# Optimization experiments

Measured on AMD Instinct MI355X. Metric: run time of the kernel, lower is better.

The kernel has to match this reference:

```python
import jax, jax.numpy as jnp
import numpy as np

NU, NI, C, E, L = 100000, 50000, 128, 1000000, 200000
TAU = 0.05  # SemanticUpdateWA weight on past embeddings


def setup_inputs() -> dict:
    key = jax.random.key(0)
    ks = jax.random.split(key, 40)
    it = iter(ks)
    f = lambda shape, s=1.0: jax.random.normal(next(it), shape, jnp.float32) * s
    inp = {}
    inp['x_user'] = f((NU, C))
    inp['x_item'] = f((NI, C))
    inp['past1_user'] = f((NU, C))
    inp['past1_item'] = f((NI, C))
    inp['past2_user'] = f((NU, C))
    inp['past2_item'] = f((NI, C))
    w = 0.05  # param scale
    for nm, shp in [('W1ui_n', (C, C)), ('W1ui_s', (C, C)), ('W1iu_n', (C, C)), ('W1iu_s', (C, C)),
                    ('Wp1', (C, C)), ('bp1', (C,)), ('Wa1', (C, C)), ('ba1', (C,)), ('q1', (C,)),
                    ('W2ui_n', (C, C)), ('W2ui_s', (C, C)), ('W2iu_n', (C, C)), ('W2iu_s', (C, C)),
                    ('Wp2', (C, C)), ('bp2', (C,)), ('Wa2', (C, C)), ('ba2', (C,)), ('q2', (C,)),
                    ('Wpost', (C, 2)), ('bpost', (2,))]:
        inp[nm] = f(shp, w)
    inp['src_ui'] = jax.random.randint(next(it), (E,), 0, NU)
    inp['dst_ui'] = jax.random.randint(next(it), (E,), 0, NI)
    inp['src_iu'] = jax.random.randint(next(it), (E,), 0, NI)
    inp['dst_iu'] = jax.random.randint(next(it), (E,), 0, NU)
    inp['lbl_src'] = jax.random.randint(next(it), (L,), 0, NU)
    inp['lbl_dst'] = jax.random.randint(next(it), (L,), 0, NI)
    inp['snap'] = 1
    return inp


def _seg_mean(src_feat, src, dst, n_dst):
    # mean-aggregated messages: gather src features along edges, scatter-mean to dst
    msg = src_feat[src]                                   # [E, C]
    s = jax.ops.segment_sum(msg, dst, num_segments=n_dst)  # [n_dst, C]
    cnt = jax.ops.segment_sum(jnp.ones((src.shape[0], 1), src_feat.dtype), dst, num_segments=n_dst)
    return s / jnp.maximum(cnt, 1.0)


def _sem_agg(z, W, b, q):
    # HAN-style semantic attention over relations. z: [N, R, C]
    w = jnp.einsum('nrc,c->nr', jnp.tanh(jnp.einsum('nrc,cd->nrd', z, W) + b), q).mean(axis=0)  # [R]
    beta = jax.nn.softmax(w)
    return jnp.einsum('nrc,r->nc', z, beta)


def reference(x_user, x_item, past1_user, past1_item, past2_user, past2_item,
              W1ui_n, W1ui_s, W1iu_n, W1iu_s, Wp1, bp1, Wa1, ba1, q1,
              W2ui_n, W2ui_s, W2iu_n, W2iu_s, Wp2, bp2, Wa2, ba2, q2,
              Wpost, bpost,
              src_ui, dst_ui, src_iu, dst_iu, lbl_src, lbl_dst, snap):
    # --- layer 1: per-relation heterogeneous conv (GraphConv-style: W_n*mean_aggr + W_s*x_self) ---
    item1 = _seg_mean(x_user, src_ui, dst_ui, NI) @ W1ui_n + x_item @ W1ui_s
    user1 = _seg_mean(x_item, src_iu, dst_iu, NU) @ W1iu_n + x_user @ W1iu_s
    user1 = user1 @ Wp1 + bp1                              # projuser1
    if snap != 0:                                          # temporal weighted-average update
        user1 = TAU * past1_user + (1.0 - TAU) * user1
        item1 = TAU * past1_item + (1.0 - TAU) * item1
    cur1_user, cur1_item = user1, item1
    user_h = _sem_agg(user1[:, None, :], Wa1, ba1, q1)     # semantic aggregation (R=1 per type)
    item_h = _sem_agg(item1[:, None, :], Wa1, ba1, q1)
    # --- layer 2 ---
    item2 = _seg_mean(user_h, src_ui, dst_ui, NI) @ W2ui_n + item_h @ W2ui_s
    user2 = _seg_mean(item_h, src_iu, dst_iu, NU) @ W2iu_n + user_h @ W2iu_s
    user2 = user2 @ Wp2 + bp2                              # projuser2
    if snap != 0:
        user2 = TAU * past2_user + (1.0 - TAU) * user2
        item2 = TAU * past2_item + (1.0 - TAU) * item2
    cur2_user, cur2_item = user2, item2
    user_o = _sem_agg(user2[:, None, :], Wa2, ba2, q2)
    item_o = _sem_agg(item2[:, None, :], Wa2, ba2, q2)
    # --- link scoring: gather, Hadamard, linear, sum ---
    h = ((user_o[lbl_src] * item_o[lbl_dst]) @ Wpost + bpost).sum(axis=-1)  # [L]
    return (h, cur1_user, cur1_item, cur2_user, cur2_item)
```

## Files before the change

kernel.cpp:

```cpp
#include <hip/hip_runtime.h>


#define NUSER 100000
#define NITEM 50000
#define CDIM  128
#define EDGES 1000000
#define LBL   200000

#define OFF_C1U ((long)LBL)
#define OFF_C1I (OFF_C1U + (long)NUSER * CDIM)
#define OFF_C2U (OFF_C1I + (long)NITEM * CDIM)
#define OFF_C2I (OFF_C2U + (long)NUSER * CDIM)

typedef __bf16 bf16x8 __attribute__((ext_vector_type(8)));
typedef float  f32x4  __attribute__((ext_vector_type(4)));

__device__ __forceinline__ float ld1(const void* base, size_t idx, bool isf32) {
  return isf32 ? ((const float*)base)[idx] : (float)((const __bf16*)base)[idx];
}

__global__ void probe_dtype_kernel(const unsigned short* __restrict__ x,
                                   int* __restrict__ flag) {
  int t = threadIdx.x;
  int bad = 0;
  for (int i = t * 2; i < 8192; i += 512) {
    int e = (x[i] >> 7) & 0xFF;
    if (e > 0x85) bad = 1;
  }
  if (bad) atomicOr(flag, 1);
}

__global__ __launch_bounds__(256) void hist_kernel(
    const int* __restrict__ dst_ui, const int* __restrict__ dst_iu,
    int* __restrict__ cntI, int* __restrict__ cntU) {
  int e = blockIdx.x * 256 + threadIdx.x;
  if (e < EDGES) {
    atomicAdd(&cntI[dst_ui[e]], 1);
    atomicAdd(&cntU[dst_iu[e]], 1);
  }
}

__global__ __launch_bounds__(1024) void scan2_kernel(
    const int* __restrict__ cntI, int* __restrict__ offI, int* __restrict__ curI,
    int nI, const int* __restrict__ cntU, int* __restrict__ offU,
    int* __restrict__ curU, int nU) {
  const int* cnt = blockIdx.x ? cntU : cntI;
  int* off = blockIdx.x ? offU : offI;
  int* cur = blockIdx.x ? curU : curI;
  int n = blockIdx.x ? nU : nI;
  __shared__ int wsums[16];
  __shared__ int carry_s;
  int t = threadIdx.x, lane = t & 63, w = t >> 6;
  if (t == 0) carry_s = 0;
  __syncthreads();
  for (int base = 0; base < n; base += 1024) {
    int i = base + t;
    int v = (i < n) ? cnt[i] : 0;
    int x = v;
#pragma unroll
    for (int s = 1; s < 64; s <<= 1) {
      int y = __shfl_up(x, s, 64);
      if (lane >= s) x += y;
    }
    if (lane == 63) wsums[w] = x;
    __syncthreads();
    int woff = 0;
    for (int ww = 0; ww < w; ++ww) woff += wsums[ww];
    int carry = carry_s;
    __syncthreads();
    int excl = carry + woff + x - v;
    if (i < n) { off[i] = excl; cur[i] = excl; }
    if (t == 1023) carry_s = excl + v;
    __syncthreads();
  }
  if (t == 0) off[n] = carry_s;
}

__global__ __launch_bounds__(256) void bucket_kernel(
    const int* __restrict__ src_ui, const int* __restrict__ dst_ui,
    const int* __restrict__ src_iu, const int* __restrict__ dst_iu,
    int* __restrict__ curI, int* __restrict__ curU,
    int* __restrict__ permI, int* __restrict__ permU) {
  int e = blockIdx.x * 256 + threadIdx.x;
  if (e < EDGES) {
    int p = atomicAdd(&curI[dst_ui[e]], 1);
    permI[p] = src_ui[e];
    int p2 = atomicAdd(&curU[dst_iu[e]], 1);
    permU[p2] = src_iu[e];
  }
}

__global__ __launch_bounds__(256) void convert_bf16_kernel(
    const void* __restrict__ in, __bf16* __restrict__ outp, long n,
    const int* __restrict__ flag) {
  bool f = flag[0] != 0;
  long i = ((long)blockIdx.x * 256 + threadIdx.x) * 8;
  if (i + 8 > n) return;
  bf16x8 o;
  if (f) {
    f32x4 a = *(const f32x4*)((const float*)in + i);
    f32x4 b = *(const f32x4*)((const float*)in + i + 4);
#pragma unroll
    for (int j = 0; j < 4; ++j) {
      o[j] = (__bf16)a[j];
      o[4 + j] = (__bf16)b[j];
    }
  } else {
    o = *(const bf16x8*)((const __bf16*)in + i);
  }
  *(bf16x8*)(outp + i) = o;
}

__global__ __launch_bounds__(128) void prep_transpose_kernel(
    const void* __restrict__ W0, const void* __restrict__ W1,
    const void* __restrict__ W2, const void* __restrict__ W3,
    __bf16* __restrict__ T0, __bf16* __restrict__ T1,
    __bf16* __restrict__ T2, __bf16* __restrict__ T3,
    const int* __restrict__ flag) {
  bool f = flag[0] != 0;
  int k = blockIdx.x, n = threadIdx.x, y = blockIdx.y;
  const void* W = (y == 0) ? W0 : (y == 1) ? W1 : (y == 2) ? W2 : W3;
  __bf16* T = (y == 0) ? T0 : (y == 1) ? T1 : (y == 2) ? T2 : T3;
  T[n * CDIM + k] = (__bf16)ld1(W, (size_t)k * CDIM + n, f);
}

__global__ __launch_bounds__(128) void prep_combine_kernel(
    const void* __restrict__ W0, const void* __restrict__ W1,
    const void* __restrict__ W2, const void* __restrict__ W3,
    const void* __restrict__ Wp1, const void* __restrict__ Wp2,
    __bf16* __restrict__ T0, __bf16* __restrict__ T1,
    __bf16* __restrict__ T2, __bf16* __restrict__ T3,
    const int* __restrict__ flag) {
  bool f = flag[0] != 0;
  int k = blockIdx.x, n = threadIdx.x, y = blockIdx.y;
  const void* W = (y == 0) ? W0 : (y == 1) ? W1 : (y == 2) ? W2 : W3;
  const void* Wp = (y < 2) ? Wp1 : Wp2;
  __bf16* T = (y == 0) ? T0 : (y == 1) ? T1 : (y == 2) ? T2 : T3;
  float s = 0.f;
#pragma unroll 4
  for (int j = 0; j < CDIM; ++j)
    s += ld1(W, (size_t)k * CDIM + j, f) * ld1(Wp, (size_t)j * CDIM + n, f);
  T[n * CDIM + k] = (__bf16)s;
}

__global__ void prep_misc_kernel(const void* __restrict__ Wpost,
                                 const void* __restrict__ bpost,
                                 const void* __restrict__ bp1,
                                 const void* __restrict__ bp2,
                                 float* __restrict__ wsum,
                                 float* __restrict__ bpf1,
                                 float* __restrict__ bpf2,
                                 const int* __restrict__ flag) {
  bool f = flag[0] != 0;
  int t = threadIdx.x;
  wsum[t] = ld1(Wpost, (size_t)t * 2, f) + ld1(Wpost, (size_t)t * 2 + 1, f);
  bpf1[t] = ld1(bp1, t, f);
  bpf2[t] = ld1(bp2, t, f);
  if (t == 0) wsum[CDIM] = ld1(bpost, 0, f) + ld1(bpost, 1, f);
}

template <bool HAS_BIAS>
__global__ __launch_bounds__(256, 4) void gather_gemm_coop(
    const int* __restrict__ off, const int* __restrict__ perm,
    const __bf16* __restrict__ feat, const __bf16* __restrict__ X,
    const __bf16* __restrict__ WtN, const __bf16* __restrict__ WtS,
    const float* __restrict__ bias, const void* __restrict__ past,
    __bf16* __restrict__ shadow_out, const int* __restrict__ snapp,
    const int* __restrict__ flag, void* __restrict__ outb, long outoff,
    int nRowTiles) {
  __shared__ float lds[4][16][132];
  float* ldsOut = &lds[0][0][0];
  bool f32o = (flag[0] != 0);
  bool blend = (snapp[0] != 0);
  int t = threadIdx.x;
  int w = t >> 6, lane = t & 63, ln = lane & 15, q = lane >> 4;
  int cq = q * 8;
  for (int rt = blockIdx.x; rt < nRowTiles; rt += gridDim.x) {
    int row = rt * 16 + ln;
    int beg = off[row], end = off[row + 1];
    int cnt = end - beg;
    int myBeg = beg + ((cnt * w) >> 2);
    int myEnd = beg + ((cnt * (w + 1)) >> 2);
    float s[4][8];
#pragma unroll
    for (int a = 0; a < 4; ++a)
#pragma unroll
      for (int j = 0; j < 8; ++j) s[a][j] = 0.f;
    {
      const __bf16* fb = feat + cq;
      int i = myBeg;
      for (; i + 1 < myEnd; i += 2) {
        const __bf16* fp0 = fb + (size_t)perm[i] * CDIM;
        const __bf16* fp1 = fb + (size_t)perm[i + 1] * CDIM;
        bf16x8 v0[4], v1[4];
#pragma unroll
        for (int ks = 0; ks < 4; ++ks) v0[ks] = *(const bf16x8*)(fp0 + ks * 32);
#pragma unroll
        for (int ks = 0; ks < 4; ++ks) v1[ks] = *(const bf16x8*)(fp1 + ks * 32);
#pragma unroll
        for (int ks = 0; ks < 4; ++ks)
#pragma unroll
          for (int j = 0; j < 8; ++j)
            s[ks][j] += (float)v0[ks][j] + (float)v1[ks][j];
      }
      if (i < myEnd) {
        const __bf16* fp = fb + (size_t)perm[i] * CDIM;
#pragma unroll
        for (int ks = 0; ks < 4; ++ks) {
          bf16x8 v = *(const bf16x8*)(fp + ks * 32);
#pragma unroll
          for (int j = 0; j < 8; ++j) s[ks][j] += (float)v[j];
        }
      }
    }
#pragma unroll
    for (int ks = 0; ks < 4; ++ks) {
      *(f32x4*)&lds[w][ln][cq + ks * 32] =
          (f32x4){s[ks][0], s[ks][1], s[ks][2], s[ks][3]};
      *(f32x4*)&lds[w][ln][cq + ks * 32 + 4] =
          (f32x4){s[ks][4], s[ks][5], s[ks][6], s[ks][7]};
    }
    __syncthreads();
    float rc = 1.0f / fmaxf((float)cnt, 1.0f);
    bf16x8 a1[4], a2[4];
#pragma unroll
    for (int ks = 0; ks < 4; ++ks) {
      f32x4 lo = (f32x4){0.f, 0.f, 0.f, 0.f};
      f32x4 hi = (f32x4){0.f, 0.f, 0.f, 0.f};
#pragma unroll
      for (int w2 = 0; w2 < 4; ++w2) {
        const float* p = &lds[w2][ln][cq + ks * 32];
        lo += *(const f32x4*)p;
        hi += *(const f32x4*)(p + 4);
      }
      bf16x8 t1;
#pragma unroll
      for (int j = 0; j < 4; ++j) {
        t1[j] = (__bf16)(lo[j] * rc);
        t1[4 + j] = (__bf16)(hi[j] * rc);
      }
      a1[ks] = t1;
      a2[ks] = *(const bf16x8*)(X + (size_t)row * CDIM + cq + ks * 32);
    }
    f32x4 d0 = (f32x4){0.f, 0.f, 0.f, 0.f};
    f32x4 d1 = (f32x4){0.f, 0.f, 0.f, 0.f};
    const __bf16* bn0 = WtN + (size_t)((2 * w) * 16 + ln) * CDIM + cq;
    const __bf16* bs0 = WtS + (size_t)((2 * w) * 16 + ln) * CDIM + cq;
#pragma unroll
    for (int ks = 0; ks < 4; ++ks) {
      d0 = __builtin_amdgcn_mfma_f32_16x16x32_bf16(
          a1[ks], *(const bf16x8*)(bn0 + ks * 32), d0, 0, 0, 0);
      d0 = __builtin_amdgcn_mfma_f32_16x16x32_bf16(
          a2[ks], *(const bf16x8*)(bs0 + ks * 32), d0, 0, 0, 0);
      d1 = __builtin_amdgcn_mfma_f32_16x16x32_bf16(
          a1[ks], *(const bf16x8*)(bn0 + 16 * CDIM + ks * 32), d1, 0, 0, 0);
      d1 = __builtin_amdgcn_mfma_f32_16x16x32_bf16(
          a2[ks], *(const bf16x8*)(bs0 + 16 * CDIM + ks * 32), d1, 0, 0, 0);
    }
    __syncthreads();
#pragma unroll
    for (int p = 0; p < 2; ++p) {
      f32x4 dd = p ? d1 : d0;
      int col = (2 * w + p) * 16 + ln;
      float bv = HAS_BIAS ? bias[col] : 0.0f;
#pragma unroll
      for (int r = 0; r < 4; ++r)
        ldsOut[(q * 4 + r) * 132 + col] = dd[r] + bv;
    }
    __syncthreads();
    {
      int orow16 = t >> 4, c0 = (t & 15) * 8;
      long orow = (long)rt * 16 + orow16;
      const float* lp = ldsOut + orow16 * 132 + c0;
      f32x4 v0 = *(const f32x4*)lp;
      f32x4 v1 = *(const f32x4*)(lp + 4);
      if (blend) {
        if (f32o) {
          const float* pp = (const float*)past + orow * CDIM + c0;
          f32x4 p0 = *(const f32x4*)pp;
          f32x4 p1 = *(const f32x4*)(pp + 4);
#pragma unroll
          for (int j = 0; j < 4; ++j) {
            v0[j] = 0.05f * p0[j] + 0.95f * v0[j];
            v1[j] = 0.05f * p1[j] + 0.95f * v1[j];
          }
        } else {
          bf16x8 pb =
              *(const bf16x8*)((const __bf16*)past + orow * CDIM + c0);
#pragma unroll
          for (int j = 0; j < 4; ++j) {
            v0[j] = 0.05f * (float)pb[j] + 0.95f * v0[j];
            v1[j] = 0.05f * (float)pb[4 + j] + 0.95f * v1[j];
          }
        }
      }
      if (shadow_out) {
        bf16x8 sh;
#pragma unroll
        for (int j = 0; j < 4; ++j) {
          sh[j] = (__bf16)v0[j];
          sh[4 + j] = (__bf16)v1[j];
        }
        *(bf16x8*)(shadow_out + orow * CDIM + c0) = sh;
      }
      if (f32o) {
        float* op = (float*)outb + outoff + orow * CDIM + c0;
        *(f32x4*)op = v0;
        *(f32x4*)(op + 4) = v1;
      } else {
        bf16x8 ob;
#pragma unroll
        for (int j = 0; j < 4; ++j) {
          ob[j] = (__bf16)v0[j];
          ob[4 + j] = (__bf16)v1[j];
        }
        *(bf16x8*)((__bf16*)outb + outoff + orow * CDIM + c0) = ob;
      }
    }
    __syncthreads();
  }
}

template <bool HAS_BIAS>
__global__ __launch_bounds__(256) void gather_gemm_kernel(
    const int* __restrict__ off, const int* __restrict__ perm,
    const void* __restrict__ featb, long featoff,
    const void* __restrict__ Xb, long xoff,
    const __bf16* __restrict__ WtN, const __bf16* __restrict__ WtS,
    const float* __restrict__ bias, const void* __restrict__ past,
    const int* __restrict__ snapp, const int* __restrict__ flag,
    void* __restrict__ outb, long outoff, int nRowTiles) {
  bool f32 = (flag[0] != 0);
  bool blend = (snapp[0] != 0);
  int lane = threadIdx.x & 63;
  int ln = lane & 15, q = lane >> 4;
  int wave = blockIdx.x * 4 + (threadIdx.x >> 6);
  int nW = gridDim.x * 4;
  size_t cq = (size_t)q * 8;
  for (int rt = wave; rt < nRowTiles; rt += nW) {
    int row = rt * 16 + ln;
    int beg = off[row], end = off[row + 1];
    float s[4][8];
#pragma unroll
    for (int a = 0; a < 4; ++a)
#pragma unroll
      for (int j = 0; j < 8; ++j) s[a][j] = 0.f;
    if (f32) {
      const float* fb = (const float*)featb + featoff + cq;
      for (int i = beg; i < end; ++i) {
        const float* fp = fb + (size_t)perm[i] * CDIM;
#pragma unroll
        for (int ks = 0; ks < 4; ++ks) {
          f32x4 lo = *(const f32x4*)(fp + ks * 32);
          f32x4 hi = *(const f32x4*)(fp + ks * 32 + 4);
#pragma unroll
          for (int j = 0; j < 4; ++j) {
            s[ks][j] += lo[j];
            s[ks][4 + j] += hi[j];
          }
        }
      }
    } else {
      const __bf16* fb = (const __bf16*)featb + featoff + cq;
      for (int i = beg; i < end; ++i) {
        const __bf16* fp = fb + (size_t)perm[i] * CDIM;
#pragma unroll
        for (int ks = 0; ks < 4; ++ks) {
          bf16x8 v = *(const bf16x8*)(fp + ks * 32);
#pragma unroll
          for (int j = 0; j < 8; ++j) s[ks][j] += (float)v[j];
        }
      }
    }
    float rc = 1.0f / fmaxf((float)(end - beg), 1.0f);
    bf16x8 a1[4], a2[4];
    size_t xb = (size_t)row * CDIM + cq;
#pragma unroll
    for (int ks = 0; ks < 4; ++ks) {
      bf16x8 t1, t2;
      if (f32) {
        const float* xp = (const float*)Xb + xoff + xb + ks * 32;
        f32x4 lo = *(const f32x4*)xp;
        f32x4 hi = *(const f32x4*)(xp + 4);
#pragma unroll
        for (int j = 0; j < 4; ++j) {
          t2[j] = (__bf16)lo[j];
          t2[4 + j] = (__bf16)hi[j];
        }
      } else {
        t2 = *(const bf16x8*)((const __bf16*)Xb + xoff + xb + ks * 32);
      }
#pragma unroll
      for (int j = 0; j < 8; ++j) t1[j] = (__bf16)(s[ks][j] * rc);
      a1[ks] = t1;
      a2[ks] = t2;
    }
    f32x4 d[8];
#pragma unroll
    for (int ct = 0; ct < 8; ++ct) d[ct] = (f32x4){0.f, 0.f, 0.f, 0.f};
#pragma unroll
    for (int ct = 0; ct < 8; ++ct) {
      const __bf16* bn = WtN + (size_t)(ct * 16 + ln) * CDIM + q * 8;
      const __bf16* bs = WtS + (size_t)(ct * 16 + ln) * CDIM + q * 8;
#pragma unroll
      for (int ks = 0; ks < 4; ++ks) {
        d[ct] = __builtin_amdgcn_mfma_f32_16x16x32_bf16(
            a1[ks], *(const bf16x8*)(bn + ks * 32), d[ct], 0, 0, 0);
        d[ct] = __builtin_amdgcn_mfma_f32_16x16x32_bf16(
            a2[ks], *(const bf16x8*)(bs + ks * 32), d[ct], 0, 0, 0);
      }
    }
#pragma unroll
    for (int ct = 0; ct < 8; ++ct) {
      int col = ct * 16 + ln;
      float bv = HAS_BIAS ? bias[col] : 0.0f;
#pragma unroll
      for (int r = 0; r < 4; ++r) {
        long orow = rt * 16 + q * 4 + r;
        float v = d[ct][r] + bv;
        if (blend)
          v = 0.05f * ld1(past, (size_t)orow * CDIM + col, f32) + 0.95f * v;
        size_t oidx = (size_t)(outoff + orow * CDIM + col);
        if (f32)
          ((float*)outb)[oidx] = v;
        else
          ((__bf16*)outb)[oidx] = (__bf16)v;
      }
    }
  }
}

__global__ __launch_bounds__(256) void score_kernel(
    void* __restrict__ outb, const int* __restrict__ ls,
    const int* __restrict__ ld, const float* __restrict__ wsum,
    const int* __restrict__ flag) {
  bool f32 = (flag[0] != 0);
  int t = blockIdx.x * blockDim.x + threadIdx.x;
  int l = t >> 4;
  if (l >= LBL) return;
  size_t c8 = (size_t)(t & 15) << 3;
  float av[8], bv[8];
  if (f32) {
    const float* u = (const float*)outb + OFF_C2U + (size_t)ls[l] * CDIM + c8;
    const float* v = (const float*)outb + OFF_C2I + (size_t)ld[l] * CDIM + c8;
    f32x4 u0 = *(const f32x4*)u, u1 = *(const f32x4*)(u + 4);
    f32x4 v0 = *(const f32x4*)v, v1 = *(const f32x4*)(v + 4);
#pragma unroll
    for (int j = 0; j < 4; ++j) {
      av[j] = u0[j]; av[4 + j] = u1[j];
      bv[j] = v0[j]; bv[4 + j] = v1[j];
    }
  } else {
    bf16x8 a = *(const bf16x8*)((const __bf16*)outb + OFF_C2U +
                                (size_t)ls[l] * CDIM + c8);
    bf16x8 b = *(const bf16x8*)((const __bf16*)outb + OFF_C2I +
                                (size_t)ld[l] * CDIM + c8);
#pragma unroll
    for (int j = 0; j < 8; ++j) { av[j] = (float)a[j]; bv[j] = (float)b[j]; }
  }
  float p = 0.f;
#pragma unroll
  for (int j = 0; j < 8; ++j) p += av[j] * bv[j] * wsum[c8 + j];
  p += __shfl_xor(p, 1, 16);
  p += __shfl_xor(p, 2, 16);
  p += __shfl_xor(p, 4, 16);
  p += __shfl_xor(p, 8, 16);
  if ((t & 15) == 0) {
    float h = p + wsum[CDIM];
    if (f32)
      ((float*)outb)[l] = h;
    else
      ((__bf16*)outb)[l] = (__bf16)h;
  }
}

extern "C" void kernel_launch(void* const* d_in, const int* in_sizes, int n_in,
                              void* d_out, int out_size, void* d_ws,
                              size_t ws_size, hipStream_t stream) {
  const void* x_user = d_in[0];
  const void* x_item = d_in[1];
  const void* past1_user = d_in[2];
  const void* past1_item = d_in[3];
  const void* past2_user = d_in[4];
  const void* past2_item = d_in[5];
  const void* W1ui_n = d_in[6];
  const void* W1ui_s = d_in[7];
  const void* W1iu_n = d_in[8];
  const void* W1iu_s = d_in[9];
  const void* Wp1 = d_in[10];
  const void* bp1 = d_in[11];
  const void* W2ui_n = d_in[15];
  const void* W2ui_s = d_in[16];
  const void* W2iu_n = d_in[17];
  const void* W2iu_s = d_in[18];
  const void* Wp2 = d_in[19];
  const void* bp2 = d_in[20];
  const void* Wpost = d_in[24];
  const void* bpost = d_in[25];
  const int* src_ui = (const int*)d_in[26];
  const int* dst_ui = (const int*)d_in[27];
  const int* src_iu = (const int*)d_in[28];
  const int* dst_iu = (const int*)d_in[29];
  const int* lbl_src = (const int*)d_in[30];
  const int* lbl_dst = (const int*)d_in[31];
  const int* snap = (const int*)d_in[32];

  size_t wo = 0;
  auto alloc = [&](size_t bytes) -> char* {
    char* p = (char*)d_ws + wo;
    wo += (bytes + 255) & ~(size_t)255;
    return p;
  };
  int* cntI = (int*)alloc(NITEM * 4);
  int* cntU = (int*)alloc(NUSER * 4);
  int* flag = (int*)alloc(256);
  size_t zeroBytes = wo;
  int* offI = (int*)alloc((NITEM + 1) * 4);
  int* offU = (int*)alloc((NUSER + 1) * 4);
  int* curI = (int*)alloc(NITEM * 4);
  int* curU = (int*)alloc(NUSER * 4);
  int* permI = (int*)alloc(EDGES * 4);
  int* permU = (int*)alloc(EDGES * 4);
  float* wsum = (float*)alloc(256 * 4);
  float* bpf1 = (float*)alloc(CDIM * 4);
  float* bpf2 = (float*)alloc(CDIM * 4);
  __bf16* wt0 = (__bf16*)alloc(8 * CDIM * CDIM * 2);
  __bf16* Wt[8];
  for (int i = 0; i < 8; ++i) Wt[i] = wt0 + (size_t)i * CDIM * CDIM;
  __bf16* xu_sh = (__bf16*)alloc((size_t)NUSER * CDIM * 2);
  __bf16* xi_sh = (__bf16*)alloc((size_t)NITEM * CDIM * 2);
  __bf16* c1u_sh = (__bf16*)alloc((size_t)NUSER * CDIM * 2);
  __bf16* c1i_sh = (__bf16*)alloc((size_t)NITEM * CDIM * 2);
  bool useShadow = (wo <= ws_size);

  const int EB = (EDGES + 255) / 256;
  const int T_ITEM = NITEM / 16;
  const int T_USER = NUSER / 16;

  hipMemsetAsync(d_ws, 0, zeroBytes, stream);
  probe_dtype_kernel<<<1, 256, 0, stream>>>((const unsigned short*)x_user,
                                            flag);

  hist_kernel<<<EB, 256, 0, stream>>>(dst_ui, dst_iu, cntI, cntU);
  scan2_kernel<<<2, 1024, 0, stream>>>(cntI, offI, curI, NITEM, cntU, offU,
                                       curU, NUSER);
  bucket_kernel<<<EB, 256, 0, stream>>>(src_ui, dst_ui, src_iu, dst_iu, curI,
                                        curU, permI, permU);

  prep_transpose_kernel<<<dim3(CDIM, 4), CDIM, 0, stream>>>(
      W1ui_n, W1ui_s, W2ui_n, W2ui_s, Wt[0], Wt[1], Wt[4], Wt[5], flag);
  prep_combine_kernel<<<dim3(CDIM, 4), CDIM, 0, stream>>>(
      W1iu_n, W1iu_s, W2iu_n, W2iu_s, Wp1, Wp2, Wt[2], Wt[3], Wt[6], Wt[7],
      flag);
  prep_misc_kernel<<<1, CDIM, 0, stream>>>(Wpost, bpost, bp1, bp2, wsum, bpf1,
                                           bpf2, flag);

  if (useShadow) {
    convert_bf16_kernel<<<(NUSER * CDIM) / 2048, 256, 0, stream>>>(
        x_user, xu_sh, (long)NUSER * CDIM, flag);
    convert_bf16_kernel<<<(NITEM * CDIM) / 2048, 256, 0, stream>>>(
        x_item, xi_sh, (long)NITEM * CDIM, flag);
    gather_gemm_coop<false><<<T_ITEM, 256, 0, stream>>>(
        offI, permI, xu_sh, xi_sh, Wt[0], Wt[1], nullptr, past1_item, c1i_sh,
        snap, flag, d_out, OFF_C1I, T_ITEM);
    gather_gemm_coop<true><<<T_USER, 256, 0, stream>>>(
        offU, permU, xi_sh, xu_sh, Wt[2], Wt[3], bpf1, past1_user, c1u_sh,
        snap, flag, d_out, OFF_C1U, T_USER);
    gather_gemm_coop<false><<<T_ITEM, 256, 0, stream>>>(
        offI, permI, c1u_sh, c1i_sh, Wt[4], Wt[5], nullptr, past2_item,
        nullptr, snap, flag, d_out, OFF_C2I, T_ITEM);
    gather_gemm_coop<true><<<T_USER, 256, 0, stream>>>(
        offU, permU, c1i_sh, c1u_sh, Wt[6], Wt[7], bpf2, past2_user, nullptr,
        snap, flag, d_out, OFF_C2U, T_USER);
  } else {
    const int G_ITEM = (T_ITEM + 3) / 4;
    const int G_USER = (T_USER + 3) / 4;
    gather_gemm_kernel<false><<<G_ITEM, 256, 0, stream>>>(
        offI, permI, x_user, 0, x_item, 0, Wt[0], Wt[1], nullptr, past1_item,
        snap, flag, d_out, OFF_C1I, T_ITEM);
    gather_gemm_kernel<true><<<G_USER, 256, 0, stream>>>(
        offU, permU, x_item, 0, x_user, 0, Wt[2], Wt[3], bpf1, past1_user,
        snap, flag, d_out, OFF_C1U, T_USER);
    gather_gemm_kernel<false><<<G_ITEM, 256, 0, stream>>>(
        offI, permI, d_out, OFF_C1U, d_out, OFF_C1I, Wt[4], Wt[5], nullptr,
        past2_item, snap, flag, d_out, OFF_C2I, T_ITEM);
    gather_gemm_kernel<true><<<G_USER, 256, 0, stream>>>(
        offU, permU, d_out, OFF_C1I, d_out, OFF_C1U, Wt[6], Wt[7], bpf2,
        past2_user, snap, flag, d_out, OFF_C2U, T_USER);
  }

  score_kernel<<<(LBL * 16) / 256, 256, 0, stream>>>(d_out, lbl_src, lbl_dst,
                                                     wsum, flag);
}
```

Baseline: 1.255 ms.

## Replace global-atomic CSR bucketing with two-pass binned partition

Builds the destination-sorted edge lists (CSR permutation) through a two-level partition. Edges are first binned by dst>>10 using shared-memory histograms and per-block offsets, with src and the low dst bits packed into one int. Each bin is then scattered to its final position using shared-memory atomics on row cursors. This replaces random global atomics and scattered writes in the bucket step with mostly local traffic, at the cost of extra passes, an extra pairs buffer and a larger scan.

```diff
diff --git a/kernel.cpp b/kernel.cpp
--- a/kernel.cpp
+++ b/kernel.cpp
@@ -6,6 +6,12 @@
 #define CDIM  128
 #define EDGES 1000000
 #define LBL   200000
+
+#define NBLK  256
+#define BINSH 10
+#define BINW  1024
+#define NBI   ((NITEM + BINW - 1) / BINW)
+#define NBU   ((NUSER + BINW - 1) / BINW)
 
 #define OFF_C1U ((long)LBL)
 #define OFF_C1I (OFF_C1U + (long)NUSER * CDIM)
@@ -30,24 +36,46 @@
   if (bad) atomicOr(flag, 1);
 }
 
-__global__ __launch_bounds__(256) void hist_kernel(
+__global__ __launch_bounds__(256) void partA_kernel(
     const int* __restrict__ dst_ui, const int* __restrict__ dst_iu,
-    int* __restrict__ cntI, int* __restrict__ cntU) {
-  int e = blockIdx.x * 256 + threadIdx.x;
-  if (e < EDGES) {
-    atomicAdd(&cntI[dst_ui[e]], 1);
-    atomicAdd(&cntU[dst_iu[e]], 1);
-  }
-}
-
-__global__ __launch_bounds__(1024) void scan2_kernel(
-    const int* __restrict__ cntI, int* __restrict__ offI, int* __restrict__ curI,
-    int nI, const int* __restrict__ cntU, int* __restrict__ offU,
-    int* __restrict__ curU, int nU) {
-  const int* cnt = blockIdx.x ? cntU : cntI;
-  int* off = blockIdx.x ? offU : offI;
-  int* cur = blockIdx.x ? curU : curI;
-  int n = blockIdx.x ? nU : nI;
+    int* __restrict__ cntI, int* __restrict__ cntU, int* __restrict__ HI,
+    int* __restrict__ HU) {
+  __shared__ int h[128];
+  int t = threadIdx.x, b = blockIdx.x, rel = blockIdx.y;
+  const int* dst = rel ? dst_iu : dst_ui;
+  int* cnt = rel ? cntU : cntI;
+  int* H = rel ? HU : HI;
+  int nbins = rel ? NBU : NBI;
+  if (t < 128) h[t] = 0;
+  __syncthreads();
+  const int chunk = (EDGES + NBLK - 1) / NBLK;
+  int beg = b * chunk;
+  int end = min(beg + chunk, EDGES);
+  for (int e = beg + t; e < end; e += 256) {
+    int d = dst[e];
+    atomicAdd(&cnt[d], 1);
+    atomicAdd(&h[d >> BINSH], 1);
+  }
+  __syncthreads();
+  if (t < nbins) H[t * NBLK + b] = h[t];
+}
+
+__global__ __launch_bounds__(1024) void scan4_kernel(
+    const int* __restrict__ c0, int* __restrict__ o0, int* __restrict__ u0,
+    int n0, const int* __restrict__ c1, int* __restrict__ o1,
+    int* __restrict__ u1, int n1, const int* __restrict__ c2,
+    int* __restrict__ o2, int n2, const int* __restrict__ c3,
+    int* __restrict__ o3, int n3) {
+  const int* cnt;
+  int* off;
+  int* cur;
+  int n;
+  switch (blockIdx.x) {
+    case 0: cnt = c0; off = o0; cur = u0; n = n0; break;
+    case 1: cnt = c1; off = o1; cur = u1; n = n1; break;
+    case 2: cnt = c2; off = o2; cur = nullptr; n = n2; break;
+    default: cnt = c3; off = o3; cur = nullptr; n = n3; break;
+  }
   __shared__ int wsums[16];
   __shared__ int carry_s;
   int t = threadIdx.x, lane = t & 63, w = t >> 6;
@@ -69,11 +97,75 @@
     int carry = carry_s;
     __syncthreads();
     int excl = carry + woff + x - v;
-    if (i < n) { off[i] = excl; cur[i] = excl; }
+    if (i < n) {
+      off[i] = excl;
+      if (cur) cur[i] = excl;
+    }
     if (t == 1023) carry_s = excl + v;
     __syncthreads();
   }
   if (t == 0) off[n] = carry_s;
+}
+
+__global__ __launch_bounds__(256) void partC_kernel(
+    const int* __restrict__ src_ui, const int* __restrict__ dst_ui,
+    const int* __restrict__ src_iu, const int* __restrict__ dst_iu,
+    const int* __restrict__ HIoff, const int* __restrict__ HUoff,
+    int* __restrict__ pairsI, int* __restrict__ pairsU) {
+  __shared__ int cur[128];
+  int t = threadIdx.x, b = blockIdx.x, rel = blockIdx.y;
+  const int* src = rel ? src_iu : src_ui;
+  const int* dst = rel ? dst_iu : dst_ui;
+  const int* Hoff = rel ? HUoff : HIoff;
+  int* pairs = rel ? pairsU : pairsI;
+  int nbins = rel ? NBU : NBI;
+  if (t < 128) cur[t] = (t < nbins) ? Hoff[t * NBLK + b] : 0;
+  __syncthreads();
+  const int chunk = (EDGES + NBLK - 1) / NBLK;
+  int beg = b * chunk;
+  int end = min(beg + chunk, EDGES);
+  for (int e = beg + t; e < end; e += 256) {
+    int d = dst[e];
+    int p = atomicAdd(&cur[d >> BINSH], 1);
+    pairs[p] = src[e] | ((d & (BINW - 1)) << 17);
+  }
+}
+
+__global__ __launch_bounds__(256) void bucketB_kernel(
+    const int* __restrict__ HIoff, const int* __restrict__ HUoff,
+    const int* __restrict__ pairsI, const int* __restrict__ pairsU,
+    const int* __restrict__ offI, const int* __restrict__ offU,
+    int* __restrict__ permI, int* __restrict__ permU) {
+  __shared__ int rcur[BINW];
+  int t = threadIdx.x, bin = blockIdx.x, rel = blockIdx.y;
+  int nbins = rel ? NBU : NBI;
+  if (bin >= nbins) return;
+  const int* Hoff = rel ? HUoff : HIoff;
+  const int* pairs = rel ? pairsU : pairsI;
+  const int* off = rel ? offU : offI;
+  int* perm = rel ? permU : permI;
+  int nrows = rel ? NUSER : NITEM;
+  int base = bin << BINSH;
+  int rows = min(BINW, nrows - base);
+  for (int i = t; i < rows; i += 256) rcur[i] = off[base + i];
+  __syncthreads();
+  int s = Hoff[bin * NBLK];
+  int e = Hoff[(bin + 1) * NBLK];
+  for (int i = s + t; i < e; i += 256) {
+    int v = pairs[i];
+    int p = atomicAdd(&rcur[v >> 17], 1);
+    perm[p] = v & 0x1FFFF;
+  }
+}
+
+__global__ __launch_bounds__(256) void hist_kernel(
+    const int* __restrict__ dst_ui, const int* __restrict__ dst_iu,
+    int* __restrict__ cntI, int* __restrict__ cntU) {
+  int e = blockIdx.x * 256 + threadIdx.x;
+  if (e < EDGES) {
+    atomicAdd(&cntI[dst_ui[e]], 1);
+    atomicAdd(&cntU[dst_iu[e]], 1);
+  }
 }
 
 __global__ __launch_bounds__(256) void bucket_kernel(
@@ -532,6 +624,13 @@
   __bf16* c1u_sh = (__bf16*)alloc((size_t)NUSER * CDIM * 2);
   __bf16* c1i_sh = (__bf16*)alloc((size_t)NITEM * CDIM * 2);
   bool useShadow = (wo <= ws_size);
+  int* HI = (int*)alloc((size_t)(NBI * NBLK + 1) * 4);
+  int* HU = (int*)alloc((size_t)(NBU * NBLK + 1) * 4);
+  int* HIoff = (int*)alloc((size_t)(NBI * NBLK + 1) * 4);
+  int* HUoff = (int*)alloc((size_t)(NBU * NBLK + 1) * 4);
+  int* pairsI = (int*)alloc((size_t)EDGES * 4);
+  int* pairsU = (int*)alloc((size_t)EDGES * 4);
+  bool usePart = (wo <= ws_size);
 
   const int EB = (EDGES + 255) / 256;
   const int T_ITEM = NITEM / 16;
@@ -541,11 +640,24 @@
   probe_dtype_kernel<<<1, 256, 0, stream>>>((const unsigned short*)x_user,
                                             flag);
 
-  hist_kernel<<<EB, 256, 0, stream>>>(dst_ui, dst_iu, cntI, cntU);
-  scan2_kernel<<<2, 1024, 0, stream>>>(cntI, offI, curI, NITEM, cntU, offU,
-                                       curU, NUSER);
-  bucket_kernel<<<EB, 256, 0, stream>>>(src_ui, dst_ui, src_iu, dst_iu, curI,
-                                        curU, permI, permU);
+  if (usePart) {
+    partA_kernel<<<dim3(NBLK, 2), 256, 0, stream>>>(dst_ui, dst_iu, cntI,
+                                                    cntU, HI, HU);
+    scan4_kernel<<<4, 1024, 0, stream>>>(cntI, offI, curI, NITEM, cntU, offU,
+                                         curU, NUSER, HI, HIoff, NBI * NBLK,
+                                         HU, HUoff, NBU * NBLK);
+    partC_kernel<<<dim3(NBLK, 2), 256, 0, stream>>>(
+        src_ui, dst_ui, src_iu, dst_iu, HIoff, HUoff, pairsI, pairsU);
+    bucketB_kernel<<<dim3(NBU, 2), 256, 0, stream>>>(
+        HIoff, HUoff, pairsI, pairsU, offI, offU, permI, permU);
+  } else {
+    hist_kernel<<<EB, 256, 0, stream>>>(dst_ui, dst_iu, cntI, cntU);
+    scan4_kernel<<<2, 1024, 0, stream>>>(cntI, offI, curI, NITEM, cntU, offU,
+                                         curU, NUSER, nullptr, nullptr, 0,
+                                         nullptr, nullptr, 0);
+    bucket_kernel<<<EB, 256, 0, stream>>>(src_ui, dst_ui, src_iu, dst_iu,
+                                          curI, curU, permI, permU);
+  }
 
   prep_transpose_kernel<<<dim3(CDIM, 4), CDIM, 0, stream>>>(
       W1ui_n, W1ui_s, W2ui_n, W2ui_s, Wt[0], Wt[1], Wt[4], Wt[5], flag);
```

Result: faster. 1.145 ms (-8.8%).
